# Kernel tuning notes

Hardware: AMD Instinct MI355X
Metric: run time of the kernel (lower is better)

## Reference

```python
import jax, jax.numpy as jnp
import numpy as np

B_SZ, SEQ, H, P = 4, 8192, 512, 256


def _s5(x, lam_re, lam_im, log_dt, b_re, b_im, c_re, c_im, d):
    """Single-direction S5 diagonal SSM. x: [B,L,H] -> y: [B,L,H]."""
    lam = lam_re + 1j * lam_im                      # [P] complex diagonal A
    dt = jnp.exp(log_dt)                            # [P] ZOH timestep
    a_bar = jnp.exp(lam * dt)                       # [P] discretized A
    b_bar = ((a_bar - 1.0) / lam)[:, None] * (b_re + 1j * b_im)  # [P,H]
    bu = jnp.einsum('blh,ph->blp', x.astype(b_bar.dtype), b_bar)  # [B,L,P]
    a_el = jnp.broadcast_to(a_bar, bu.shape)        # time-invariant A per step

    def comb(e1, e2):  # associative combine for linear recurrence
        a1, s1 = e1
        a2, s2 = e2
        return (a1 * a2, a2 * s1 + s2)

    _, states = jax.lax.associative_scan(comb, (a_el, bu), axis=1)  # [B,L,P]
    c = c_re + 1j * c_im                            # [H,P]
    return jnp.einsum('blp,hp->blh', states, c).real + x * d


def setup_inputs() -> dict:
    key = jax.random.key(0)
    ks = jax.random.split(key, 10)
    return {
        'x': jax.random.normal(ks[0], (B_SZ, SEQ, H), dtype=jnp.float32),
        'Lambda_re': -0.1 - 0.5 * jax.random.uniform(ks[1], (2, P), dtype=jnp.float32),
        'Lambda_im': jnp.pi * jax.random.normal(ks[2], (2, P), dtype=jnp.float32),
        'log_dt': jnp.log(0.001) + (jnp.log(0.1) - jnp.log(0.001)) * jax.random.uniform(ks[3], (2, P), dtype=jnp.float32),
        'B_re': jax.random.normal(ks[4], (2, P, H), dtype=jnp.float32) / np.sqrt(H),
        'B_im': jax.random.normal(ks[5], (2, P, H), dtype=jnp.float32) / np.sqrt(H),
        'C_re': jax.random.normal(ks[6], (2, H, P), dtype=jnp.float32) / np.sqrt(P),
        'C_im': jax.random.normal(ks[7], (2, H, P), dtype=jnp.float32) / np.sqrt(P),
        'D': jax.random.normal(ks[8], (2, H), dtype=jnp.float32),
    }


def reference(x, Lambda_re, Lambda_im, log_dt, B_re, B_im, C_re, C_im, D):
    # fwd(x) + flip(bwd(flip(x)))
    y_f = _s5(x, Lambda_re[0], Lambda_im[0], log_dt[0], B_re[0], B_im[0], C_re[0], C_im[0], D[0])
    x_r = x[:, ::-1]
    y_b = _s5(x_r, Lambda_re[1], Lambda_im[1], log_dt[1], B_re[1], B_im[1], C_re[1], C_im[1], D[1])[:, ::-1]
    return y_f + y_b
```

## Files before the change

### kernel.cpp

```cpp
#include <hip/hip_runtime.h>
#include <math.h>

typedef unsigned short ushort_t;
typedef __bf16 bf16x8 __attribute__((ext_vector_type(8)));
typedef ushort_t ushort8v __attribute__((ext_vector_type(8)));
typedef float f32x4 __attribute__((ext_vector_type(4)));

#define B_SZ   4
#define SEQ    8192
#define M_ROWS (B_SZ * SEQ)
#define CH     128
#define NC     (SEQ / CH)

__device__ __forceinline__ ushort_t f2bf(float f) {
    unsigned u = __float_as_uint(f);
    u = u + 0x7fffu + ((u >> 16) & 1u);
    return (ushort_t)(u >> 16);
}
__device__ __forceinline__ float bf2f(ushort_t b) {
    return __uint_as_float(((unsigned)b) << 16);
}

__device__ __forceinline__ void load16_lds(const void* g, void* l) {
    __builtin_amdgcn_global_load_lds(
        (const __attribute__((address_space(1))) unsigned int*)g,
        (__attribute__((address_space(3))) unsigned int*)l, 16, 0, 0);
}

__device__ __forceinline__ bf16x8 ldfrag(const ushort_t* p) {
    union { ushort8v u; bf16x8 b; } cv;
    cv.u = *(const ushort8v*)p;
    return cv.b;
}

__device__ __forceinline__ float2 cmul(float2 a, float2 b) {
    return make_float2(a.x * b.x - a.y * b.y, a.x * b.y + a.y * b.x);
}

__global__ void prepconv_kernel(const float* __restrict__ x,
                                ushort_t* __restrict__ X16,
                                const float* __restrict__ Lre,
                                const float* __restrict__ Lim,
                                const float* __restrict__ ldt,
                                const float* __restrict__ Bre,
                                const float* __restrict__ Bim,
                                const float* __restrict__ Cre,
                                const float* __restrict__ Cim,
                                float* __restrict__ abar,
                                float* __restrict__ apow,
                                float* __restrict__ PW,
                                ushort_t* __restrict__ Bmat,
                                ushort_t* __restrict__ Cmat) {
    int i = blockIdx.x * 256 + threadIdx.x;
    float4 v = ((const float4*)x)[i];
    ushort_t o[4] = {f2bf(v.x), f2bf(v.y), f2bf(v.z), f2bf(v.w)};
    *(uint2*)&X16[(size_t)i * 4] = *(const uint2*)o;

    if (blockIdx.x < 1024) {
        int idx = i;
        int h = idx & 511;
        int p = (idx >> 9) & 255;
        int d = idx >> 17;
        int ip = d * 256 + p;
        float lr = Lre[ip], li = Lim[ip];
        float dt = expf(ldt[ip]);
        float e   = expf(lr * dt);
        float ang = li * dt;
        float ar = e * cosf(ang), ai = e * sinf(ang);
        float nr = ar - 1.0f, ni = ai;
        float den = lr * lr + li * li;
        float cr = (nr * lr + ni * li) / den;
        float ci = (ni * lr - nr * li) / den;
        float br = Bre[idx], bi = Bim[idx];
        Bmat[(d * 512 + 2 * p) * 512 + h]     = f2bf(cr * br - ci * bi);
        Bmat[(d * 512 + 2 * p + 1) * 512 + h] = f2bf(cr * bi + ci * br);
        if (h == 0) {
            int oo = d * 512 + 2 * p;
            abar[oo] = ar;  abar[oo + 1] = ai;
            float eC = expf(lr * dt * (float)CH);
            float aC = ang * (float)CH;
            apow[oo] = eC * cosf(aC);  apow[oo + 1] = eC * sinf(aC);
            float2 a1 = make_float2(ar, ai);
            float2 a2 = cmul(a1, a1);
            float2 a4 = cmul(a2, a2);
            float2 a8 = cmul(a4, a4);
            float2 a16 = cmul(a8, a8);
            int q = d * 256 + p;
            PW[q * 6 + 0] = a1.x;  PW[q * 6 + 1] = a1.y;
            PW[q * 6 + 2] = a4.x;  PW[q * 6 + 3] = a4.y;
            PW[q * 6 + 4] = a16.x; PW[q * 6 + 5] = a16.y;
        }
        int p2 = idx & 255;
        int h2 = (idx >> 8) & 511;
        int d2 = idx >> 17;
        Cmat[h2 * 1024 + d2 * 512 + 2 * p2]     = f2bf(Cre[idx]);
        Cmat[h2 * 1024 + d2 * 512 + 2 * p2 + 1] = f2bf(-Cim[idx]);
    }
}

template<int EPI, int KD_, int NT>
__global__ __launch_bounds__(512, 2)
void gemm_8ph(const ushort_t* __restrict__ A, const ushort_t* __restrict__ Bm,
              ushort_t* __restrict__ Cb, float* __restrict__ Cf,
              const float* __restrict__ X, const float* __restrict__ Dv,
              const float* __restrict__ PW, float* __restrict__ CAR) {
    __shared__ ushort_t shA[2][2][256 * 32];
    __shared__ ushort_t shB[2][2][256 * 32];
    constexpr int NKT = KD_ / 64;

    const int tid  = threadIdx.x;
    const int lane = tid & 63;
    const int wv   = tid >> 6;
    const int wr = wv >> 2, wc = wv & 3;
    const int l15 = lane & 15, lq = lane >> 4;

    const int lin = blockIdx.x;
    const int xcd = lin & 7;
    const int j   = lin >> 3;
    const int mt  = xcd * 16 + j / NT;
    const int nt  = j % NT;
    const int m0 = mt * 256;
    const int n0 = nt * 256;
    const int CN = NT * 256;

    f32x4 acc[8][4];
#pragma unroll
    for (int i = 0; i < 8; ++i)
#pragma unroll
        for (int jj = 0; jj < 4; ++jj)
            acc[i][jj] = (f32x4){0.f, 0.f, 0.f, 0.f};

    const int srow = wv * 32 + (lane >> 2);
    const int sck  = (((lane & 3) ^ ((lane >> 3) & 3))) * 8;
    const ushort_t* Ag = A  + (size_t)(m0 + srow) * KD_ + sck;
    const ushort_t* Bg = Bm + (size_t)(n0 + srow) * KD_ + sck;

#define STAGE_A(t, ks) do {                                                   \
        const ushort_t* g_ = Ag + (size_t)(t) * 64 + (ks) * 32;               \
        ushort_t* d_ = &shA[(t) & 1][(ks)][wv * 1024];                        \
        load16_lds(g_, d_);                                                   \
        load16_lds(g_ + (size_t)16 * KD_, d_ + 512);                          \
    } while (0)
#define STAGE_B(t, ks) do {                                                   \
        const ushort_t* g_ = Bg + (size_t)(t) * 64 + (ks) * 32;               \
        ushort_t* d_ = &shB[(t) & 1][(ks)][wv * 1024];                        \
        load16_lds(g_, d_);                                                   \
        load16_lds(g_ + (size_t)16 * KD_, d_ + 512);                          \
    } while (0)

    const int rdoff = ((lq ^ ((l15 >> 1) & 3))) * 8;
    const int rdA = (wr * 128 + l15) * 32 + rdoff;
    const int rdB = (wc * 64  + l15) * 32 + rdoff;

#define MFMA_PH(bx, by, nlo) do {                                             \
        __builtin_amdgcn_s_setprio(1);                                        \
        _Pragma("unroll")                                                     \
        for (int mi_ = 0; mi_ < 8; ++mi_) {                                   \
            acc[mi_][nlo]     = __builtin_amdgcn_mfma_f32_16x16x32_bf16(      \
                af[mi_], bx, acc[mi_][nlo], 0, 0, 0);                         \
            acc[mi_][nlo + 1] = __builtin_amdgcn_mfma_f32_16x16x32_bf16(      \
                af[mi_], by, acc[mi_][nlo + 1], 0, 0, 0);                     \
        }                                                                     \
        __builtin_amdgcn_s_setprio(0);                                        \
    } while (0)

    STAGE_A(0, 0); STAGE_A(0, 1); STAGE_B(0, 0); STAGE_B(0, 1);
    STAGE_A(1, 0); STAGE_B(1, 0); STAGE_A(1, 1);
    asm volatile("s_waitcnt vmcnt(6)" ::: "memory");
    __builtin_amdgcn_s_barrier();

    bf16x8 af[8];
#pragma unroll 2
    for (int kt = 0; kt < NKT; ++kt) {
        const int buf = kt & 1;
        const ushort_t* aS0 = &shA[buf][0][rdA];
        const ushort_t* aS1 = &shA[buf][1][rdA];
        const ushort_t* bS0 = &shB[buf][0][rdB];
        const ushort_t* bS1 = &shB[buf][1][rdB];

        {
#pragma unroll
            for (int mi = 0; mi < 8; ++mi) af[mi] = ldfrag(aS0 + mi * 512);
            bf16x8 b0 = ldfrag(bS0), b1 = ldfrag(bS0 + 512);
            if (kt + 1 < NKT) STAGE_B(kt + 1, 1);
            __builtin_amdgcn_s_barrier();
            MFMA_PH(b0, b1, 0);
            __builtin_amdgcn_s_barrier();
        }
        {
            bf16x8 b2 = ldfrag(bS0 + 1024), b3 = ldfrag(bS0 + 1536);
            if (kt + 2 < NKT) STAGE_A(kt + 2, 0);
            __builtin_amdgcn_s_barrier();
            MFMA_PH(b2, b3, 2);
            __builtin_amdgcn_s_barrier();
        }
        {
#pragma unroll
            for (int mi = 0; mi < 8; ++mi) af[mi] = ldfrag(aS1 + mi * 512);
            bf16x8 b0 = ldfrag(bS1), b1 = ldfrag(bS1 + 512);
            if (kt + 2 < NKT) STAGE_B(kt + 2, 0);
            __builtin_amdgcn_s_barrier();
            MFMA_PH(b0, b1, 0);
            __builtin_amdgcn_s_barrier();
        }
        {
            bf16x8 b2 = ldfrag(bS1 + 1024), b3 = ldfrag(bS1 + 1536);
            if (kt + 2 < NKT) STAGE_A(kt + 2, 1);
            __builtin_amdgcn_s_barrier();
            MFMA_PH(b2, b3, 2);
            if (kt + 1 < NKT) {
                if (kt + 2 < NKT)
                    asm volatile("s_waitcnt vmcnt(6)" ::: "memory");
                else
                    asm volatile("s_waitcnt vmcnt(0)" ::: "memory");
                __builtin_amdgcn_s_barrier();
            }
        }
    }
#undef STAGE_A
#undef STAGE_B
#undef MFMA_PH

    asm volatile("s_waitcnt lgkmcnt(0)" ::: "memory");
    __builtin_amdgcn_s_barrier();

    const int rr = lane >> 2;
    const int cc = (lane & 3) * 16;

    if (EPI == 0) {
        ushort_t* ep = (ushort_t*)((char*)shA + wv * 2304);
#pragma unroll
        for (int mi = 0; mi < 8; ++mi) {
#pragma unroll
            for (int ni = 0; ni < 4; ++ni)
#pragma unroll
                for (int r = 0; r < 4; ++r)
                    ep[(lq * 4 + r) * 72 + ni * 16 + l15] = f2bf(acc[mi][ni][r]);
            uint4 w0 = *(const uint4*)&ep[rr * 72 + cc];
            uint4 w1 = *(const uint4*)&ep[rr * 72 + cc + 8];
            const int rowg = m0 + wr * 128 + mi * 16 + rr;
            *(uint4*)&Cb[(size_t)rowg * CN + n0 + wc * 64 + cc]     = w0;
            *(uint4*)&Cb[(size_t)rowg * CN + n0 + wc * 64 + cc + 8] = w1;
        }
    } else {
        float* epf = (float*)((char*)shA + wv * 4352);
        const int colbase = n0 + wc * 64 + cc;
        f32x4 dsv[4];
#pragma unroll
        for (int j4 = 0; j4 < 4; ++j4)
            dsv[j4] = *(const f32x4*)&Dv[colbase + j4 * 4]
                    + *(const f32x4*)&Dv[512 + colbase + j4 * 4];
#pragma unroll
        for (int mi = 0; mi < 8; ++mi) {
#pragma unroll
            for (int ni = 0; ni < 4; ++ni)
#pragma unroll
                for (int r = 0; r < 4; ++r)
                    epf[(lq * 4 + r) * 68 + ni * 16 + l15] = acc[mi][ni][r];
            const int rowg = m0 + wr * 128 + mi * 16 + rr;
            const size_t gb = (size_t)rowg * 512 + colbase;
#pragma unroll
            for (int j4 = 0; j4 < 4; ++j4) {
                f32x4 v  = *(const f32x4*)&epf[rr * 68 + cc + j4 * 4];
                f32x4 xv = *(const f32x4*)&X[gb + j4 * 4];
                v = v + xv * dsv[j4];
                *(f32x4*)&Cf[gb + j4 * 4] = v;
            }
        }
    }

    if (EPI == 0) {
        const int dirq = n0 >> 9;
        const bool evn = ((l15 & 1) == 0);
        const int cidx = ((m0 >> 7) + wr) * 1024;

#define CACC(MI, R, CC) do {                                                  \
            float vo = bf2f(f2bf(acc[MI][ni][R]));                            \
            float vp = __shfl_xor(vo, 1);                                     \
            float vr = evn ? vo : vp;                                         \
            float vi = evn ? vp : vo;                                         \
            wr_ = fmaf(CC.x, vr, fmaf(-CC.y, vi, wr_));                       \
            wi_ = fmaf(CC.x, vi, fmaf(CC.y, vr, wi_));                        \
        } while (0)
#define CSTEP(MI) do {                                                        \
            float wr_ = 0.f, wi_ = 0.f;                                       \
            CACC(MI, 0, c0); CACC(MI, 1, c1);                                 \
            CACC(MI, 2, c2); CACC(MI, 3, c3);                                 \
            float comp = evn ? (t16.x * wr_ - t16.y * wi_)                    \
                             : (t16.x * wi_ + t16.y * wr_);                   \
            csum += comp;                                                     \
            t16 = cmul(t16, A16);                                             \
        } while (0)

#pragma unroll
        for (int ni = 0; ni < 4; ++ni) {
            const int col = n0 + wc * 64 + ni * 16 + l15;
            const int q = col >> 1;
            float2 A1  = make_float2(PW[q * 6 + 0], PW[q * 6 + 1]);
            float2 A4  = make_float2(PW[q * 6 + 2], PW[q * 6 + 3]);
            float2 A16 = make_float2(PW[q * 6 + 4], PW[q * 6 + 5]);
            const int lqp = dirq ? lq : 3 - lq;
            float2 A4_2 = cmul(A4, A4);
            float2 A4_3 = cmul(A4_2, A4);
            float2 P4 = (lqp == 0) ? make_float2(1.f, 0.f)
                       : (lqp == 1) ? A4
                       : (lqp == 2) ? A4_2 : A4_3;
            float2 c0, c1, c2, c3;
            if (dirq == 0) {
                c3 = P4; c2 = cmul(c3, A1); c1 = cmul(c2, A1); c0 = cmul(c1, A1);
            } else {
                c0 = P4; c1 = cmul(c0, A1); c2 = cmul(c1, A1); c3 = cmul(c2, A1);
            }
            float2 t16 = make_float2(1.f, 0.f);
            float csum = 0.f;
            if (dirq == 0) {
                CSTEP(7); CSTEP(6); CSTEP(5); CSTEP(4);
                CSTEP(3); CSTEP(2); CSTEP(1); CSTEP(0);
            } else {
                CSTEP(0); CSTEP(1); CSTEP(2); CSTEP(3);
                CSTEP(4); CSTEP(5); CSTEP(6); CSTEP(7);
            }
            csum += __shfl_xor(csum, 16);
            csum += __shfl_xor(csum, 32);
            if (lq == 0) CAR[cidx + col] = csum;
        }
#undef CACC
#undef CSTEP
    }
}

__global__ __launch_bounds__(512)
void scan_fin2(ushort_t* __restrict__ S, const float* __restrict__ abar,
               const float* __restrict__ apow, const float* __restrict__ carry) {
    int b = blockIdx.x, c = blockIdx.y, t = threadIdx.x;
    int dir = t >> 8, p = t & 255;
    float ar = abar[dir * 512 + 2 * p], ai = abar[dir * 512 + 2 * p + 1];
    float pr = apow[dir * 512 + 2 * p], pi = apow[dir * 512 + 2 * p + 1];
    float sr = 0.f, si = 0.f;
    if (dir == 0) {
        for (int cc = 0; cc < c; ++cc) {
            int o = (b * NC + cc) * 1024 + 2 * p;
            float cr0 = carry[o], ci0 = carry[o + 1];
            float nr = fmaf(pr, sr, fmaf(-pi, si, cr0));
            float ni = fmaf(pr, si, fmaf(pi, sr, ci0));
            sr = nr; si = ni;
        }
    } else {
        for (int cc = NC - 1; cc > c; --cc) {
            int o = (b * NC + cc) * 1024 + 512 + 2 * p;
            float cr0 = carry[o], ci0 = carry[o + 1];
            float nr = fmaf(pr, sr, fmaf(-pi, si, cr0));
            float ni = fmaf(pr, si, fmaf(pi, sr, ci0));
            sr = nr; si = ni;
        }
    }
    ushort_t* base = S + ((size_t)b * SEQ + (size_t)c * CH) * 1024
                       + dir * 512 + 2 * p;
    for (int ii = 0; ii < CH; ++ii) {
        int i = dir ? (CH - 1 - ii) : ii;
        unsigned* addr = (unsigned*)(base + (size_t)i * 1024);
        unsigned u = *addr;
        float re = bf2f((ushort_t)(u & 0xffffu));
        float im = bf2f((ushort_t)(u >> 16));
        float nr = fmaf(ar, sr, fmaf(-ai, si, re));
        float ni = fmaf(ar, si, fmaf(ai, sr, im));
        sr = nr; si = ni;
        *addr = ((unsigned)f2bf(si) << 16) | (unsigned)f2bf(sr);
    }
}

extern "C" void kernel_launch(void* const* d_in, const int* in_sizes, int n_in,
                              void* d_out, int out_size, void* d_ws, size_t ws_size,
                              hipStream_t stream) {
    const float* x   = (const float*)d_in[0];
    const float* Lre = (const float*)d_in[1];
    const float* Lim = (const float*)d_in[2];
    const float* ldt = (const float*)d_in[3];
    const float* Bre = (const float*)d_in[4];
    const float* Bim = (const float*)d_in[5];
    const float* Cre = (const float*)d_in[6];
    const float* Cim = (const float*)d_in[7];
    const float* Dv  = (const float*)d_in[8];
    float* y = (float*)d_out;
    char* ws = (char*)d_ws;

    ushort_t* SB16 = (ushort_t*)(ws);
    ushort_t* X16  = (ushort_t*)(ws + 67108864);
    ushort_t* Bm16 = (ushort_t*)(ws + 100663296);
    ushort_t* Cm16 = (ushort_t*)(ws + 101711872);
    float* abar  = (float*)(ws + 102760448);
    float* apow  = (float*)(ws + 102764544);
    float* carry = (float*)d_out;
    float* PW    = (float*)((char*)d_out + 1048576);

    prepconv_kernel<<<16384, 256, 0, stream>>>(x, X16, Lre, Lim, ldt,
                                               Bre, Bim, Cre, Cim,
                                               abar, apow, PW, Bm16, Cm16);

    gemm_8ph<0, 512, 4><<<512, 512, 0, stream>>>(X16, Bm16, SB16, nullptr,
                                                 nullptr, nullptr, PW, carry);

    dim3 gs(B_SZ, NC);
    scan_fin2<<<gs, 512, 0, stream>>>(SB16, abar, apow, carry);

    gemm_8ph<1, 1024, 2><<<256, 512, 0, stream>>>(SB16, Cm16, nullptr, y,
                                                  x, Dv, nullptr, nullptr);
}
```

Measured before the change: 273.4 us.

## Shrink GEMM tiles to 128x256 with BK32 and combine chunk carries in LDS

Replaces the 256x256, BK64 eight-phase GEMM with a 128x256 tile using a BK32 double-buffered pipeline. This doubles the grid and raises launch bounds to allow four blocks per CU, aiming for more occupancy and latency hiding. Because each 128-row chunk is now split across two wave rows of 64, the chunk-carry epilogue combines the two half-chunk partial sums through LDS using a new precomputed a^64 power. The cost is more redundant global reads of B per output and extra epilogue synchronization.

```diff
diff --git a/kernel.cpp b/kernel.cpp
--- a/kernel.cpp
+++ b/kernel.cpp
@@ -85,10 +85,13 @@
             float2 a4 = cmul(a2, a2);
             float2 a8 = cmul(a4, a4);
             float2 a16 = cmul(a8, a8);
+            float2 a32 = cmul(a16, a16);
+            float2 a64 = cmul(a32, a32);
             int q = d * 256 + p;
-            PW[q * 6 + 0] = a1.x;  PW[q * 6 + 1] = a1.y;
-            PW[q * 6 + 2] = a4.x;  PW[q * 6 + 3] = a4.y;
-            PW[q * 6 + 4] = a16.x; PW[q * 6 + 5] = a16.y;
+            PW[q * 8 + 0] = a1.x;  PW[q * 8 + 1] = a1.y;
+            PW[q * 8 + 2] = a4.x;  PW[q * 8 + 3] = a4.y;
+            PW[q * 8 + 4] = a16.x; PW[q * 8 + 5] = a16.y;
+            PW[q * 8 + 6] = a64.x; PW[q * 8 + 7] = a64.y;
         }
         int p2 = idx & 255;
         int h2 = (idx >> 8) & 511;
@@ -99,14 +102,15 @@
 }
 
 template<int EPI, int KD_, int NT>
-__global__ __launch_bounds__(512, 2)
-void gemm_8ph(const ushort_t* __restrict__ A, const ushort_t* __restrict__ Bm,
-              ushort_t* __restrict__ Cb, float* __restrict__ Cf,
-              const float* __restrict__ X, const float* __restrict__ Dv,
-              const float* __restrict__ PW, float* __restrict__ CAR) {
-    __shared__ ushort_t shA[2][2][256 * 32];
-    __shared__ ushort_t shB[2][2][256 * 32];
-    constexpr int NKT = KD_ / 64;
+__global__ __launch_bounds__(512, 4)
+void gemm_bk32(const ushort_t* __restrict__ A, const ushort_t* __restrict__ Bm,
+               ushort_t* __restrict__ Cb, float* __restrict__ Cf,
+               const float* __restrict__ X, const float* __restrict__ Dv,
+               const float* __restrict__ PW, float* __restrict__ CAR) {
+    __shared__ char smem[49152];
+    ushort_t (*shA)[4096] = (ushort_t(*)[4096])smem;
+    ushort_t (*shB)[8192] = (ushort_t(*)[8192])(smem + 16384);
+    constexpr int NKT = KD_ / 32;
 
     const int tid  = threadIdx.x;
     const int lane = tid & 63;
@@ -117,109 +121,69 @@
     const int lin = blockIdx.x;
     const int xcd = lin & 7;
     const int j   = lin >> 3;
-    const int mt  = xcd * 16 + j / NT;
+    const int mt  = xcd * 32 + j / NT;
     const int nt  = j % NT;
-    const int m0 = mt * 256;
+    const int m0 = mt * 128;
     const int n0 = nt * 256;
     const int CN = NT * 256;
 
-    f32x4 acc[8][4];
-#pragma unroll
-    for (int i = 0; i < 8; ++i)
+    f32x4 acc[4][4];
+#pragma unroll
+    for (int i = 0; i < 4; ++i)
 #pragma unroll
         for (int jj = 0; jj < 4; ++jj)
             acc[i][jj] = (f32x4){0.f, 0.f, 0.f, 0.f};
 
-    const int srow = wv * 32 + (lane >> 2);
-    const int sck  = (((lane & 3) ^ ((lane >> 3) & 3))) * 8;
-    const ushort_t* Ag = A  + (size_t)(m0 + srow) * KD_ + sck;
-    const ushort_t* Bg = Bm + (size_t)(n0 + srow) * KD_ + sck;
-
-#define STAGE_A(t, ks) do {                                                   \
-        const ushort_t* g_ = Ag + (size_t)(t) * 64 + (ks) * 32;               \
-        ushort_t* d_ = &shA[(t) & 1][(ks)][wv * 1024];                        \
-        load16_lds(g_, d_);                                                   \
-        load16_lds(g_ + (size_t)16 * KD_, d_ + 512);                          \
+    const int srA = wv * 16 + (lane >> 2);
+    const int srB = wv * 32 + (lane >> 2);
+    const int sck = (((lane & 3) ^ ((lane >> 3) & 3))) * 8;
+    const ushort_t* Ag = A  + (size_t)(m0 + srA) * KD_ + sck;
+    const ushort_t* Bg = Bm + (size_t)(n0 + srB) * KD_ + sck;
+
+#define STAGE(t) do {                                                         \
+        load16_lds(Ag + (size_t)(t) * 32, &shA[(t) & 1][wv * 512]);           \
+        load16_lds(Bg + (size_t)(t) * 32, &shB[(t) & 1][wv * 1024]);          \
+        load16_lds(Bg + (size_t)(t) * 32 + (size_t)16 * KD_,                  \
+                   &shB[(t) & 1][wv * 1024 + 512]);                           \
     } while (0)
-#define STAGE_B(t, ks) do {                                                   \
-        const ushort_t* g_ = Bg + (size_t)(t) * 64 + (ks) * 32;               \
-        ushort_t* d_ = &shB[(t) & 1][(ks)][wv * 1024];                        \
-        load16_lds(g_, d_);                                                   \
-        load16_lds(g_ + (size_t)16 * KD_, d_ + 512);                          \
-    } while (0)
 
     const int rdoff = ((lq ^ ((l15 >> 1) & 3))) * 8;
-    const int rdA = (wr * 128 + l15) * 32 + rdoff;
-    const int rdB = (wc * 64  + l15) * 32 + rdoff;
-
-#define MFMA_PH(bx, by, nlo) do {                                             \
-        __builtin_amdgcn_s_setprio(1);                                        \
-        _Pragma("unroll")                                                     \
-        for (int mi_ = 0; mi_ < 8; ++mi_) {                                   \
-            acc[mi_][nlo]     = __builtin_amdgcn_mfma_f32_16x16x32_bf16(      \
-                af[mi_], bx, acc[mi_][nlo], 0, 0, 0);                         \
-            acc[mi_][nlo + 1] = __builtin_amdgcn_mfma_f32_16x16x32_bf16(      \
-                af[mi_], by, acc[mi_][nlo + 1], 0, 0, 0);                     \
-        }                                                                     \
-        __builtin_amdgcn_s_setprio(0);                                        \
-    } while (0)
-
-    STAGE_A(0, 0); STAGE_A(0, 1); STAGE_B(0, 0); STAGE_B(0, 1);
-    STAGE_A(1, 0); STAGE_B(1, 0); STAGE_A(1, 1);
-    asm volatile("s_waitcnt vmcnt(6)" ::: "memory");
+    const int rdA = (wr * 64 + l15) * 32 + rdoff;
+    const int rdB = (wc * 64 + l15) * 32 + rdoff;
+
+    STAGE(0); STAGE(1);
+    asm volatile("s_waitcnt vmcnt(3)" ::: "memory");
     __builtin_amdgcn_s_barrier();
 
-    bf16x8 af[8];
 #pragma unroll 2
     for (int kt = 0; kt < NKT; ++kt) {
         const int buf = kt & 1;
-        const ushort_t* aS0 = &shA[buf][0][rdA];
-        const ushort_t* aS1 = &shA[buf][1][rdA];
-        const ushort_t* bS0 = &shB[buf][0][rdB];
-        const ushort_t* bS1 = &shB[buf][1][rdB];
-
-        {
-#pragma unroll
-            for (int mi = 0; mi < 8; ++mi) af[mi] = ldfrag(aS0 + mi * 512);
-            bf16x8 b0 = ldfrag(bS0), b1 = ldfrag(bS0 + 512);
-            if (kt + 1 < NKT) STAGE_B(kt + 1, 1);
+        bf16x8 af[4], bq[4];
+#pragma unroll
+        for (int mi = 0; mi < 4; ++mi)
+            af[mi] = ldfrag(&shA[buf][rdA + mi * 512]);
+#pragma unroll
+        for (int ni = 0; ni < 4; ++ni)
+            bq[ni] = ldfrag(&shB[buf][rdB + ni * 512]);
+        __builtin_amdgcn_s_barrier();
+        if (kt + 2 < NKT) STAGE(kt + 2);
+        __builtin_amdgcn_s_setprio(1);
+#pragma unroll
+        for (int mi = 0; mi < 4; ++mi)
+#pragma unroll
+            for (int ni = 0; ni < 4; ++ni)
+                acc[mi][ni] = __builtin_amdgcn_mfma_f32_16x16x32_bf16(
+                    af[mi], bq[ni], acc[mi][ni], 0, 0, 0);
+        __builtin_amdgcn_s_setprio(0);
+        if (kt + 1 < NKT) {
+            if (kt + 2 < NKT)
+                asm volatile("s_waitcnt vmcnt(3)" ::: "memory");
+            else
+                asm volatile("s_waitcnt vmcnt(0)" ::: "memory");
             __builtin_amdgcn_s_barrier();
-            MFMA_PH(b0, b1, 0);
-            __builtin_amdgcn_s_barrier();
-        }
-        {
-            bf16x8 b2 = ldfrag(bS0 + 1024), b3 = ldfrag(bS0 + 1536);
-            if (kt + 2 < NKT) STAGE_A(kt + 2, 0);
-            __builtin_amdgcn_s_barrier();
-            MFMA_PH(b2, b3, 2);
-            __builtin_amdgcn_s_barrier();
-        }
-        {
-#pragma unroll
-            for (int mi = 0; mi < 8; ++mi) af[mi] = ldfrag(aS1 + mi * 512);
-            bf16x8 b0 = ldfrag(bS1), b1 = ldfrag(bS1 + 512);
-            if (kt + 2 < NKT) STAGE_B(kt + 2, 0);
-            __builtin_amdgcn_s_barrier();
-            MFMA_PH(b0, b1, 0);
-            __builtin_amdgcn_s_barrier();
-        }
-        {
-            bf16x8 b2 = ldfrag(bS1 + 1024), b3 = ldfrag(bS1 + 1536);
-            if (kt + 2 < NKT) STAGE_A(kt + 2, 1);
-            __builtin_amdgcn_s_barrier();
-            MFMA_PH(b2, b3, 2);
-            if (kt + 1 < NKT) {
-                if (kt + 2 < NKT)
-                    asm volatile("s_waitcnt vmcnt(6)" ::: "memory");
-                else
-                    asm volatile("s_waitcnt vmcnt(0)" ::: "memory");
-                __builtin_amdgcn_s_barrier();
-            }
-        }
-    }
-#undef STAGE_A
-#undef STAGE_B
-#undef MFMA_PH
+        }
+    }
+#undef STAGE
 
     asm volatile("s_waitcnt lgkmcnt(0)" ::: "memory");
     __builtin_amdgcn_s_barrier();
@@ -228,9 +192,9 @@
     const int cc = (lane & 3) * 16;
 
     if (EPI == 0) {
-        ushort_t* ep = (ushort_t*)((char*)shA + wv * 2304);
-#pragma unroll
-        for (int mi = 0; mi < 8; ++mi) {
+        ushort_t* ep = (ushort_t*)(smem + wv * 2304);
+#pragma unroll
+        for (int mi = 0; mi < 4; ++mi) {
 #pragma unroll
             for (int ni = 0; ni < 4; ++ni)
 #pragma unroll
@@ -238,12 +202,12 @@
                     ep[(lq * 4 + r) * 72 + ni * 16 + l15] = f2bf(acc[mi][ni][r]);
             uint4 w0 = *(const uint4*)&ep[rr * 72 + cc];
             uint4 w1 = *(const uint4*)&ep[rr * 72 + cc + 8];
-            const int rowg = m0 + wr * 128 + mi * 16 + rr;
+            const int rowg = m0 + wr * 64 + mi * 16 + rr;
             *(uint4*)&Cb[(size_t)rowg * CN + n0 + wc * 64 + cc]     = w0;
             *(uint4*)&Cb[(size_t)rowg * CN + n0 + wc * 64 + cc + 8] = w1;
         }
     } else {
-        float* epf = (float*)((char*)shA + wv * 4352);
+        float* epf = (float*)(smem + wv * 4352);
         const int colbase = n0 + wc * 64 + cc;
         f32x4 dsv[4];
 #pragma unroll
@@ -251,13 +215,13 @@
             dsv[j4] = *(const f32x4*)&Dv[colbase + j4 * 4]
                     + *(const f32x4*)&Dv[512 + colbase + j4 * 4];
 #pragma unroll
-        for (int mi = 0; mi < 8; ++mi) {
+        for (int mi = 0; mi < 4; ++mi) {
 #pragma unroll
             for (int ni = 0; ni < 4; ++ni)
 #pragma unroll
                 for (int r = 0; r < 4; ++r)
                     epf[(lq * 4 + r) * 68 + ni * 16 + l15] = acc[mi][ni][r];
-            const int rowg = m0 + wr * 128 + mi * 16 + rr;
+            const int rowg = m0 + wr * 64 + mi * 16 + rr;
             const size_t gb = (size_t)rowg * 512 + colbase;
 #pragma unroll
             for (int j4 = 0; j4 < 4; ++j4) {
@@ -270,17 +234,18 @@
     }
 
     if (EPI == 0) {
-        const int dirq = n0 >> 9;
+        float* PLDS = (float*)(smem + 20480);
+        const int dirq = ((n0 + wc * 64) >> 9) & 1;
         const bool evn = ((l15 & 1) == 0);
-        const int cidx = ((m0 >> 7) + wr) * 1024;
-
-#define CACC(MI, R, CC) do {                                                  \
+        float csA[4], cpA[4], a64x[4], a64y[4];
+
+#define CACC(MI, R, CCo) do {                                                 \
             float vo = bf2f(f2bf(acc[MI][ni][R]));                            \
             float vp = __shfl_xor(vo, 1);                                     \
             float vr = evn ? vo : vp;                                         \
             float vi = evn ? vp : vo;                                         \
-            wr_ = fmaf(CC.x, vr, fmaf(-CC.y, vi, wr_));                       \
-            wi_ = fmaf(CC.x, vi, fmaf(CC.y, vr, wi_));                        \
+            wr_ = fmaf(CCo.x, vr, fmaf(-CCo.y, vi, wr_));                     \
+            wi_ = fmaf(CCo.x, vi, fmaf(CCo.y, vr, wi_));                      \
         } while (0)
 #define CSTEP(MI) do {                                                        \
             float wr_ = 0.f, wi_ = 0.f;                                       \
@@ -296,9 +261,10 @@
         for (int ni = 0; ni < 4; ++ni) {
             const int col = n0 + wc * 64 + ni * 16 + l15;
             const int q = col >> 1;
-            float2 A1  = make_float2(PW[q * 6 + 0], PW[q * 6 + 1]);
-            float2 A4  = make_float2(PW[q * 6 + 2], PW[q * 6 + 3]);
-            float2 A16 = make_float2(PW[q * 6 + 4], PW[q * 6 + 5]);
+            float2 A1  = make_float2(PW[q * 8 + 0], PW[q * 8 + 1]);
+            float2 A4  = make_float2(PW[q * 8 + 2], PW[q * 8 + 3]);
+            float2 A16 = make_float2(PW[q * 8 + 4], PW[q * 8 + 5]);
+            a64x[ni] = PW[q * 8 + 6]; a64y[ni] = PW[q * 8 + 7];
             const int lqp = dirq ? lq : 3 - lq;
             float2 A4_2 = cmul(A4, A4);
             float2 A4_3 = cmul(A4_2, A4);
@@ -313,16 +279,35 @@
             }
             float2 t16 = make_float2(1.f, 0.f);
             float csum = 0.f;
-            if (dirq == 0) {
-                CSTEP(7); CSTEP(6); CSTEP(5); CSTEP(4);
-                CSTEP(3); CSTEP(2); CSTEP(1); CSTEP(0);
-            } else {
-                CSTEP(0); CSTEP(1); CSTEP(2); CSTEP(3);
-                CSTEP(4); CSTEP(5); CSTEP(6); CSTEP(7);
-            }
+            if (dirq == 0) { CSTEP(3); CSTEP(2); CSTEP(1); CSTEP(0); }
+            else           { CSTEP(0); CSTEP(1); CSTEP(2); CSTEP(3); }
             csum += __shfl_xor(csum, 16);
             csum += __shfl_xor(csum, 32);
-            if (lq == 0) CAR[cidx + col] = csum;
+            csA[ni] = csum;
+            cpA[ni] = __shfl_xor(csum, 1);
+            if (lq == 0)
+                PLDS[wr * 256 + wc * 64 + ni * 16 + l15] = csum;
+        }
+        __builtin_amdgcn_s_barrier();
+        if (wr == 0) {
+#pragma unroll
+            for (int ni = 0; ni < 4; ++ni) {
+                const int cl = wc * 64 + ni * 16 + l15;
+                float oth_same = PLDS[256 + cl];
+                float oth_part = PLDS[256 + (cl ^ 1)];
+                float own_re = evn ? csA[ni] : cpA[ni];
+                float own_im = evn ? cpA[ni] : csA[ni];
+                float oth_re = evn ? oth_same : oth_part;
+                float oth_im = evn ? oth_part : oth_same;
+                float Xre = dirq ? oth_re : own_re;
+                float Xim = dirq ? oth_im : own_im;
+                float Ysm = dirq ? csA[ni] : oth_same;
+                float out = evn
+                    ? fmaf(a64x[ni], Xre, fmaf(-a64y[ni], Xim, Ysm))
+                    : fmaf(a64x[ni], Xim, fmaf( a64y[ni], Xre, Ysm));
+                if (lq == 0)
+                    CAR[(size_t)(m0 >> 7) * 1024 + n0 + cl] = out;
+            }
         }
 #undef CACC
 #undef CSTEP
@@ -397,12 +382,12 @@
                                                Bre, Bim, Cre, Cim,
                                                abar, apow, PW, Bm16, Cm16);
 
-    gemm_8ph<0, 512, 4><<<512, 512, 0, stream>>>(X16, Bm16, SB16, nullptr,
-                                                 nullptr, nullptr, PW, carry);
+    gemm_bk32<0, 512, 4><<<1024, 512, 0, stream>>>(X16, Bm16, SB16, nullptr,
+                                                   nullptr, nullptr, PW, carry);
 
     dim3 gs(B_SZ, NC);
     scan_fin2<<<gs, 512, 0, stream>>>(SB16, abar, apow, carry);
 
-    gemm_8ph<1, 1024, 2><<<256, 512, 0, stream>>>(SB16, Cm16, nullptr, y,
-                                                  x, Dv, nullptr, nullptr);
-}
+    gemm_bk32<1, 1024, 2><<<512, 512, 0, stream>>>(SB16, Cm16, nullptr, y,
+                                                   x, Dv, nullptr, nullptr);
+}
```

New measurement: 279.8 us. 2.3% more time.
